# Optimization experiments

Measured on AMD Instinct MI355X. Metric: run time of the kernel, lower is better.

## Reference

```python
import jax, jax.numpy as jnp
import numpy as np

D_MODEL = 1024
N_HEADS = 16
HEAD_DIM = D_MODEL // N_HEADS


def setup_inputs() -> dict:
    key = jax.random.key(0)
    ks = jax.random.split(key, 12)
    B, S = 1, 4096
    s = 1.0 / np.sqrt(D_MODEL)
    return {
        "query": jax.random.normal(ks[0], (B, S, D_MODEL), jnp.float32),
        "key": jax.random.normal(ks[1], (B, S, D_MODEL), jnp.float32),
        "value": jax.random.normal(ks[2], (B, S, D_MODEL), jnp.float32),
        "attention_mask": jnp.ones((B, S), jnp.int32),
        "Wq": jax.random.normal(ks[3], (D_MODEL, D_MODEL), jnp.float32) * s,
        "bq": jax.random.normal(ks[4], (D_MODEL,), jnp.float32) * s,
        "Wk": jax.random.normal(ks[5], (D_MODEL, D_MODEL), jnp.float32) * s,
        "bk": jax.random.normal(ks[6], (D_MODEL,), jnp.float32) * s,
        "Wv": jax.random.normal(ks[7], (D_MODEL, D_MODEL), jnp.float32) * s,
        "bv": jax.random.normal(ks[8], (D_MODEL,), jnp.float32) * s,
        "Wo": jax.random.normal(ks[9], (D_MODEL, D_MODEL), jnp.float32) * s,
        "bo": jax.random.normal(ks[10], (D_MODEL,), jnp.float32) * s,
    }


def reference(query, key, value, attention_mask, Wq, bq, Wk, bk, Wv, bv, Wo, bo):
    B = query.shape[0]

    def split_heads(x):  # [B,S,D] -> [B,H,S,Dh]
        return x.reshape(B, -1, N_HEADS, HEAD_DIM).transpose(0, 2, 1, 3)

    q = split_heads(query @ Wq + bq)
    k = split_heads(key @ Wk + bk)
    v = split_heads(value @ Wv + bv)

    scores = jnp.einsum("bhqd,bhkd->bhqk", q, k) / np.sqrt(HEAD_DIM)
    # 2D mask [B, Skv] -> [B,1,1,Skv]; 0 positions filled with -1e9
    mask = attention_mask[:, None, None, :]
    scores = jnp.where(mask == 0, jnp.float32(-1e9), scores)
    weights = jax.nn.softmax(scores, axis=-1)
    out = jnp.einsum("bhqk,bhkd->bhqd", weights, v)
    out = out.transpose(0, 2, 1, 3).reshape(B, -1, D_MODEL)
    return out @ Wo + bo
```

## Files before the change

kernel.cpp:

```cpp
#include <hip/hip_runtime.h>
#include <hip/hip_bf16.h>
#include <cstdint>

typedef __attribute__((ext_vector_type(8))) short short8;
typedef __attribute__((ext_vector_type(4))) float floatx4;
typedef unsigned short u16;

#define D_MODEL 1024
#define S_LEN 4096
#define N_HEADS 16
#define HEAD_DIM 64

__device__ __forceinline__ u16 f2bf(float x) {
    union { float f; uint32_t u; } v; v.f = x;
    uint32_t u = v.u;
    u += 0x7fffu + ((u >> 16) & 1u);
    return (u16)(u >> 16);
}

__device__ __forceinline__ void load_lds16(const u16* g, u16* l) {
    __builtin_amdgcn_global_load_lds(
        (const __attribute__((address_space(1))) uint32_t*)g,
        (__attribute__((address_space(3))) uint32_t*)l, 16, 0, 0);
}

struct Conv3 { const float* s[3]; u16* d[3]; };
__global__ __launch_bounds__(256) void convert3(Conv3 a, int n4) {
    const int z = blockIdx.y;
    const float* __restrict__ src = a.s[z];
    u16* __restrict__ dst = a.d[z];
    int i = blockIdx.x * 256 + threadIdx.x;
    if (i >= n4) return;
    float4 v = reinterpret_cast<const float4*>(src)[i];
    ushort4 o;
    o.x = f2bf(v.x); o.y = f2bf(v.y); o.z = f2bf(v.z); o.w = f2bf(v.w);
    reinterpret_cast<ushort4*>(dst)[i] = o;
}

struct Tr4 { const float* s[4]; u16* d[4]; };
__global__ __launch_bounds__(256) void transpose4(Tr4 a, int R, int C) {
    __shared__ u16 tile[32][34];
    const int z = blockIdx.z;
    const float* __restrict__ in = a.s[z];
    u16* __restrict__ out = a.d[z];
    const int tx = threadIdx.x, ty = threadIdx.y;
    const int c0 = blockIdx.x * 32, r0 = blockIdx.y * 32;
    #pragma unroll
    for (int j = 0; j < 32; j += 8)
        tile[ty + j][tx] = f2bf(in[(size_t)(r0 + ty + j) * C + c0 + tx]);
    __syncthreads();
    #pragma unroll
    for (int j = 0; j < 32; j += 8)
        out[(size_t)(c0 + ty + j) * R + r0 + tx] = tile[tx][ty + j];
}

template <typename OutT>
__device__ __forceinline__ void gemm_bt_core(const u16* __restrict__ A, const u16* __restrict__ Bt,
                                             const float* __restrict__ bias, OutT* __restrict__ C,
                                             int M, int N, int K, int bx, int by, int trC) {
    constexpr int LDT = 72;
    __shared__ u16 As[128 * LDT];
    __shared__ u16 Bs[128 * LDT];
    const int tid = threadIdx.x;
    const int wave = tid >> 6, lane = tid & 63;
    const int quad = lane >> 4, n16 = lane & 15;
    const int wm = wave >> 1, wn = wave & 1;
    const int m0 = by * 128, n0 = bx * 128;

    floatx4 acc[4][4];
    #pragma unroll
    for (int i = 0; i < 4; ++i)
        #pragma unroll
        for (int t = 0; t < 4; ++t) acc[i][t] = (floatx4)0.f;

    for (int kt = 0; kt < K; kt += 64) {
        __syncthreads();
        #pragma unroll
        for (int u = 0; u < 4; ++u) {
            const int c = tid + u * 256;
            const int row = c >> 3, off = (c & 7) * 8;
            *reinterpret_cast<float4*>(&As[row * LDT + off]) =
                *reinterpret_cast<const float4*>(&A[(size_t)(m0 + row) * K + kt + off]);
            *reinterpret_cast<float4*>(&Bs[row * LDT + off]) =
                *reinterpret_cast<const float4*>(&Bt[(size_t)(n0 + row) * K + kt + off]);
        }
        __syncthreads();
        #pragma unroll
        for (int kk = 0; kk < 2; ++kk) {
            short8 a[4], b[4];
            #pragma unroll
            for (int i = 0; i < 4; ++i)
                a[i] = *reinterpret_cast<const short8*>(&As[(wm * 64 + i * 16 + n16) * LDT + kk * 32 + quad * 8]);
            #pragma unroll
            for (int t = 0; t < 4; ++t)
                b[t] = *reinterpret_cast<const short8*>(&Bs[(wn * 64 + t * 16 + n16) * LDT + kk * 32 + quad * 8]);
            #pragma unroll
            for (int i = 0; i < 4; ++i)
                #pragma unroll
                for (int t = 0; t < 4; ++t)
                    acc[i][t] = __builtin_amdgcn_mfma_f32_16x16x32_bf16(a[i], b[t], acc[i][t], 0, 0, 0);
        }
    }
    #pragma unroll
    for (int t = 0; t < 4; ++t) {
        const int col = n0 + wn * 64 + t * 16 + n16;
        const float bv = bias[col];
        #pragma unroll
        for (int i = 0; i < 4; ++i) {
            #pragma unroll
            for (int r = 0; r < 4; ++r) {
                const int row = m0 + wm * 64 + i * 16 + quad * 4 + r;
                const float val = acc[i][t][r] + bv;
                const size_t idx = trC ? ((size_t)col * M + row) : ((size_t)row * N + col);
                if constexpr (sizeof(OutT) == 2) C[idx] = f2bf(val);
                else                             C[idx] = val;
            }
        }
    }
}

struct QkvArgs {
    const u16* A[3]; const u16* B[3]; const float* bias[3]; u16* C[3];
};

__global__ __launch_bounds__(256) void gemm_qkv(QkvArgs args, int M, int N, int K) {
    const int z = blockIdx.z;
    gemm_bt_core<u16>(args.A[z], args.B[z], args.bias[z], args.C[z], M, N, K,
                      blockIdx.x, blockIdx.y, z == 2 ? 1 : 0);
}

__global__ __launch_bounds__(256) void gemm_out(const u16* __restrict__ A, const u16* __restrict__ Bt,
                                                const float* __restrict__ bias, float* __restrict__ C,
                                                int M, int N, int K) {
    gemm_bt_core<float>(A, Bt, bias, C, M, N, K, blockIdx.x, blockIdx.y, 0);
}

#define LDP 72
__global__ __launch_bounds__(256) void flash_attn(const u16* __restrict__ Q, const u16* __restrict__ Kb,
                                                  const u16* __restrict__ Vt, const int* __restrict__ mask,
                                                  u16* __restrict__ O) {
    __shared__ u16 Ks[2][64 * 64];
    __shared__ u16 Vs[2][64 * 64];
    __shared__ u16 Ps[4][16 * LDP];
    const int tid = threadIdx.x;
    const int wave = tid >> 6, lane = tid & 63;
    const int quad = lane >> 4, n16 = lane & 15;
    const int bid = blockIdx.x;
    const int h = (bid & 7) * 2 + ((bid >> 3) & 1);
    const int qt = bid >> 4;
    const int hd = h * HEAD_DIM;
    const int q0 = qt * 64 + wave * 16;

    const int rl = lane >> 3, cl = lane & 7;

    short8 b_q[2];
    #pragma unroll
    for (int kk = 0; kk < 2; ++kk)
        b_q[kk] = *reinterpret_cast<const short8*>(
            &Q[(size_t)(q0 + n16) * D_MODEL + hd + kk * 32 + quad * 8]);

    float l_i = 0.f;
    floatx4 o_acc[4];
    #pragma unroll
    for (int t = 0; t < 4; ++t) o_acc[t] = (floatx4)0.f;

    #pragma unroll
    for (int u = 0; u < 2; ++u) {
        const int r = wave * 16 + u * 8 + rl;
        const int c = cl ^ (r & 7);
        load_lds16(&Kb[(size_t)(0 + r) * D_MODEL + hd + c * 8], &Ks[0][(wave * 16 + u * 8) * 64]);
        load_lds16(&Vt[(size_t)(hd + r) * S_LEN + 0 + c * 8], &Vs[0][(wave * 16 + u * 8) * 64]);
    }

    for (int it = 0; it < 64; ++it) {
        const int cur = it & 1;
        const int k0 = it * 64;
        __syncthreads();

        const int kn = ((it + 1) & 63) * 64;
        #pragma unroll
        for (int u = 0; u < 2; ++u) {
            const int r = wave * 16 + u * 8 + rl;
            const int c = cl ^ (r & 7);
            load_lds16(&Kb[(size_t)(kn + r) * D_MODEL + hd + c * 8],
                       &Ks[cur ^ 1][(wave * 16 + u * 8) * 64]);
            load_lds16(&Vt[(size_t)(hd + r) * S_LEN + kn + c * 8],
                       &Vs[cur ^ 1][(wave * 16 + u * 8) * 64]);
        }

        floatx4 s[4];
        #pragma unroll
        for (int t = 0; t < 4; ++t) {
            s[t] = (floatx4)0.f;
            #pragma unroll
            for (int kk = 0; kk < 2; ++kk) {
                const int sw = ((kk * 4 + quad) ^ (n16 & 7)) * 8;
                short8 ak = *reinterpret_cast<const short8*>(&Ks[cur][(t * 16 + n16) * 64 + sw]);
                s[t] = __builtin_amdgcn_mfma_f32_16x16x32_bf16(ak, b_q[kk], s[t], 0, 0, 0);
            }
        }
        #pragma unroll
        for (int t = 0; t < 4; ++t) {
            const int4 mv = *reinterpret_cast<const int4*>(&mask[k0 + t * 16 + quad * 4]);
            const float p0 = __expf(fmaf(s[t][0], 0.125f, mv.x == 0 ? -1.0e9f : 0.f));
            const float p1 = __expf(fmaf(s[t][1], 0.125f, mv.y == 0 ? -1.0e9f : 0.f));
            const float p2 = __expf(fmaf(s[t][2], 0.125f, mv.z == 0 ? -1.0e9f : 0.f));
            const float p3 = __expf(fmaf(s[t][3], 0.125f, mv.w == 0 ? -1.0e9f : 0.f));
            l_i += (p0 + p1) + (p2 + p3);
            union { __hip_bfloat162 h; uint32_t u; } pa, pb;
            pa.h = __float22bfloat162_rn(make_float2(p0, p1));
            pb.h = __float22bfloat162_rn(make_float2(p2, p3));
            uint2 w; w.x = pa.u; w.y = pb.u;
            *reinterpret_cast<uint2*>(&Ps[wave][n16 * LDP + t * 16 + quad * 4]) = w;
        }
        asm volatile("s_waitcnt lgkmcnt(0)" ::: "memory");
        short8 ap[2];
        #pragma unroll
        for (int kkv = 0; kkv < 2; ++kkv)
            ap[kkv] = *reinterpret_cast<const short8*>(&Ps[wave][n16 * LDP + kkv * 32 + quad * 8]);
        asm volatile("" ::: "memory");
        #pragma unroll
        for (int t = 0; t < 4; ++t) {
            #pragma unroll
            for (int kkv = 0; kkv < 2; ++kkv) {
                const int sw = ((kkv * 4 + quad) ^ (n16 & 7)) * 8;
                short8 bv = *reinterpret_cast<const short8*>(&Vs[cur][(t * 16 + n16) * 64 + sw]);
                o_acc[t] = __builtin_amdgcn_mfma_f32_16x16x32_bf16(ap[kkv], bv, o_acc[t], 0, 0, 0);
            }
        }
    }
    float lt = l_i;
    lt += __shfl_xor(lt, 16);
    lt += __shfl_xor(lt, 32);
    const float inv_l = 1.f / lt;
    float lir[4];
    #pragma unroll
    for (int r = 0; r < 4; ++r) lir[r] = __shfl(inv_l, quad * 4 + r);
    #pragma unroll
    for (int t = 0; t < 4; ++t)
        #pragma unroll
        for (int r = 0; r < 4; ++r)
            O[(size_t)(q0 + quad * 4 + r) * D_MODEL + hd + t * 16 + n16] =
                f2bf(o_acc[t][r] * lir[r]);
}

extern "C" void kernel_launch(void* const* d_in, const int* in_sizes, int n_in,
                              void* d_out, int out_size, void* d_ws, size_t ws_size,
                              hipStream_t stream) {
    const float* query = (const float*)d_in[0];
    const float* key   = (const float*)d_in[1];
    const float* value = (const float*)d_in[2];
    const int*   mask  = (const int*)d_in[3];
    const float* Wq = (const float*)d_in[4];
    const float* bq = (const float*)d_in[5];
    const float* Wk = (const float*)d_in[6];
    const float* bk = (const float*)d_in[7];
    const float* Wv = (const float*)d_in[8];
    const float* bv = (const float*)d_in[9];
    const float* Wo = (const float*)d_in[10];
    const float* bo = (const float*)d_in[11];
    float* out = (float*)d_out;

    char* ws = (char*)d_ws;
    const size_t SZ_SD = (size_t)S_LEN * D_MODEL * 2;
    const size_t SZ_W  = (size_t)D_MODEL * D_MODEL * 2;
    u16* qb  = (u16*)(ws);
    u16* kb  = (u16*)(ws + SZ_SD);
    u16* vb  = (u16*)(ws + 2 * SZ_SD);
    u16* Wqt = (u16*)(ws + 3 * SZ_SD);
    u16* Wkt = (u16*)(ws + 3 * SZ_SD + SZ_W);
    u16* Wvt = (u16*)(ws + 3 * SZ_SD + 2 * SZ_W);
    u16* Wot = (u16*)(ws + 3 * SZ_SD + 3 * SZ_W);
    u16* Qp  = (u16*)(ws + 3 * SZ_SD + 4 * SZ_W);
    u16* Kp  = (u16*)(ws + 4 * SZ_SD + 4 * SZ_W);
    u16* Vpt = (u16*)(ws + 5 * SZ_SD + 4 * SZ_W);
    u16* Oa  = kb;

    const int n4 = S_LEN * D_MODEL / 4;
    Conv3 cv;
    cv.s[0] = query; cv.s[1] = key; cv.s[2] = value;
    cv.d[0] = qb;    cv.d[1] = kb;  cv.d[2] = vb;
    convert3<<<dim3(n4 / 256, 3), 256, 0, stream>>>(cv, n4);

    Tr4 tr;
    tr.s[0] = Wq; tr.s[1] = Wk; tr.s[2] = Wv; tr.s[3] = Wo;
    tr.d[0] = Wqt; tr.d[1] = Wkt; tr.d[2] = Wvt; tr.d[3] = Wot;
    transpose4<<<dim3(32, 32, 4), dim3(32, 8), 0, stream>>>(tr, D_MODEL, D_MODEL);

    QkvArgs qa;
    qa.A[0] = qb;  qa.A[1] = kb;  qa.A[2] = vb;
    qa.B[0] = Wqt; qa.B[1] = Wkt; qa.B[2] = Wvt;
    qa.bias[0] = bq; qa.bias[1] = bk; qa.bias[2] = bv;
    qa.C[0] = Qp; qa.C[1] = Kp; qa.C[2] = Vpt;
    gemm_qkv<<<dim3(8, 32, 3), 256, 0, stream>>>(qa, S_LEN, D_MODEL, D_MODEL);

    flash_attn<<<dim3(1024), 256, 0, stream>>>(Qp, Kp, Vpt, mask, Oa);

    gemm_out<<<dim3(8, 32), 256, 0, stream>>>(Oa, Wot, bo, out, S_LEN, D_MODEL, D_MODEL);
}
```

Baseline: 344.4 us.

## Swizzle GEMM and P tiles, async LDS loads, precomputed additive mask with exp2

The GEMM core now stages A/B tiles into unpadded, XOR-swizzled LDS through direct global-to-LDS loads instead of register round-trips. Flash attention writes and reads its P buffer with the same swizzle rather than padding, and unrolls the loop by two so the double-buffer index is a compile-time constant. A small new kernel turns the integer mask into an additive float mask, so the attention loop does one fma plus a hardware exp2 with the log2e folded into the scale. The aim is fewer LDS bank conflicts, less register staging, and cheaper softmax math, at the cost of one extra tiny launch.

```diff
diff --git a/kernel.cpp b/kernel.cpp
--- a/kernel.cpp
+++ b/kernel.cpp
@@ -10,6 +10,7 @@
 #define S_LEN 4096
 #define N_HEADS 16
 #define HEAD_DIM 64
+#define SCALE_LOG2E 0.18033688f
 
 __device__ __forceinline__ u16 f2bf(float x) {
     union { float f; uint32_t u; } v; v.f = x;
@@ -37,6 +38,19 @@
     reinterpret_cast<ushort4*>(dst)[i] = o;
 }
 
+__global__ __launch_bounds__(256) void mask_to_madd(const int* __restrict__ m,
+                                                    float* __restrict__ o, int n4) {
+    int i = blockIdx.x * 256 + threadIdx.x;
+    if (i >= n4) return;
+    int4 mv = reinterpret_cast<const int4*>(m)[i];
+    float4 f;
+    f.x = mv.x == 0 ? -1.0e30f : 0.f;
+    f.y = mv.y == 0 ? -1.0e30f : 0.f;
+    f.z = mv.z == 0 ? -1.0e30f : 0.f;
+    f.w = mv.w == 0 ? -1.0e30f : 0.f;
+    reinterpret_cast<float4*>(o)[i] = f;
+}
+
 struct Tr4 { const float* s[4]; u16* d[4]; };
 __global__ __launch_bounds__(256) void transpose4(Tr4 a, int R, int C) {
     __shared__ u16 tile[32][34];
@@ -58,14 +72,14 @@
 __device__ __forceinline__ void gemm_bt_core(const u16* __restrict__ A, const u16* __restrict__ Bt,
                                              const float* __restrict__ bias, OutT* __restrict__ C,
                                              int M, int N, int K, int bx, int by, int trC) {
-    constexpr int LDT = 72;
-    __shared__ u16 As[128 * LDT];
-    __shared__ u16 Bs[128 * LDT];
+    __shared__ u16 As[128 * 64];
+    __shared__ u16 Bs[128 * 64];
     const int tid = threadIdx.x;
     const int wave = tid >> 6, lane = tid & 63;
     const int quad = lane >> 4, n16 = lane & 15;
     const int wm = wave >> 1, wn = wave & 1;
     const int m0 = by * 128, n0 = bx * 128;
+    const int rl = lane >> 3, cl = lane & 7;
 
     floatx4 acc[4][4];
     #pragma unroll
@@ -77,23 +91,27 @@
         __syncthreads();
         #pragma unroll
         for (int u = 0; u < 4; ++u) {
-            const int c = tid + u * 256;
-            const int row = c >> 3, off = (c & 7) * 8;
-            *reinterpret_cast<float4*>(&As[row * LDT + off]) =
-                *reinterpret_cast<const float4*>(&A[(size_t)(m0 + row) * K + kt + off]);
-            *reinterpret_cast<float4*>(&Bs[row * LDT + off]) =
-                *reinterpret_cast<const float4*>(&Bt[(size_t)(n0 + row) * K + kt + off]);
+            const int r = wave * 32 + u * 8 + rl;
+            const int c = cl ^ (rl & 7);
+            load_lds16(&A[(size_t)(m0 + r) * K + kt + c * 8], &As[(wave * 32 + u * 8) * 64]);
+            load_lds16(&Bt[(size_t)(n0 + r) * K + kt + c * 8], &Bs[(wave * 32 + u * 8) * 64]);
         }
         __syncthreads();
         #pragma unroll
         for (int kk = 0; kk < 2; ++kk) {
             short8 a[4], b[4];
             #pragma unroll
-            for (int i = 0; i < 4; ++i)
-                a[i] = *reinterpret_cast<const short8*>(&As[(wm * 64 + i * 16 + n16) * LDT + kk * 32 + quad * 8]);
-            #pragma unroll
-            for (int t = 0; t < 4; ++t)
-                b[t] = *reinterpret_cast<const short8*>(&Bs[(wn * 64 + t * 16 + n16) * LDT + kk * 32 + quad * 8]);
+            for (int i = 0; i < 4; ++i) {
+                const int row = wm * 64 + i * 16 + n16;
+                const int sw = ((kk * 4 + quad) ^ (n16 & 7)) * 8;
+                a[i] = *reinterpret_cast<const short8*>(&As[row * 64 + sw]);
+            }
+            #pragma unroll
+            for (int t = 0; t < 4; ++t) {
+                const int row = wn * 64 + t * 16 + n16;
+                const int sw = ((kk * 4 + quad) ^ (n16 & 7)) * 8;
+                b[t] = *reinterpret_cast<const short8*>(&Bs[row * 64 + sw]);
+            }
             #pragma unroll
             for (int i = 0; i < 4; ++i)
                 #pragma unroll
@@ -135,13 +153,13 @@
     gemm_bt_core<float>(A, Bt, bias, C, M, N, K, blockIdx.x, blockIdx.y, 0);
 }
 
-#define LDP 72
 __global__ __launch_bounds__(256) void flash_attn(const u16* __restrict__ Q, const u16* __restrict__ Kb,
-                                                  const u16* __restrict__ Vt, const int* __restrict__ mask,
+                                                  const u16* __restrict__ Vt,
+                                                  const float* __restrict__ madd,
                                                   u16* __restrict__ O) {
     __shared__ u16 Ks[2][64 * 64];
     __shared__ u16 Vs[2][64 * 64];
-    __shared__ u16 Ps[4][16 * LDP];
+    __shared__ u16 Ps[4][16 * 64];
     const int tid = threadIdx.x;
     const int wave = tid >> 6, lane = tid & 63;
     const int quad = lane >> 4, n16 = lane & 15;
@@ -152,6 +170,7 @@
     const int q0 = qt * 64 + wave * 16;
 
     const int rl = lane >> 3, cl = lane & 7;
+    const int swz = n16 & 7;
 
     short8 b_q[2];
     #pragma unroll
@@ -167,65 +186,73 @@
     #pragma unroll
     for (int u = 0; u < 2; ++u) {
         const int r = wave * 16 + u * 8 + rl;
-        const int c = cl ^ (r & 7);
-        load_lds16(&Kb[(size_t)(0 + r) * D_MODEL + hd + c * 8], &Ks[0][(wave * 16 + u * 8) * 64]);
-        load_lds16(&Vt[(size_t)(hd + r) * S_LEN + 0 + c * 8], &Vs[0][(wave * 16 + u * 8) * 64]);
+        const int c = cl ^ (rl & 7);
+        load_lds16(&Kb[(size_t)r * D_MODEL + hd + c * 8], &Ks[0][(wave * 16 + u * 8) * 64]);
+        load_lds16(&Vt[(size_t)(hd + r) * S_LEN + c * 8], &Vs[0][(wave * 16 + u * 8) * 64]);
     }
 
-    for (int it = 0; it < 64; ++it) {
-        const int cur = it & 1;
-        const int k0 = it * 64;
-        __syncthreads();
-
-        const int kn = ((it + 1) & 63) * 64;
-        #pragma unroll
-        for (int u = 0; u < 2; ++u) {
-            const int r = wave * 16 + u * 8 + rl;
-            const int c = cl ^ (r & 7);
-            load_lds16(&Kb[(size_t)(kn + r) * D_MODEL + hd + c * 8],
-                       &Ks[cur ^ 1][(wave * 16 + u * 8) * 64]);
-            load_lds16(&Vt[(size_t)(hd + r) * S_LEN + kn + c * 8],
-                       &Vs[cur ^ 1][(wave * 16 + u * 8) * 64]);
-        }
-
-        floatx4 s[4];
-        #pragma unroll
-        for (int t = 0; t < 4; ++t) {
-            s[t] = (floatx4)0.f;
-            #pragma unroll
-            for (int kk = 0; kk < 2; ++kk) {
-                const int sw = ((kk * 4 + quad) ^ (n16 & 7)) * 8;
-                short8 ak = *reinterpret_cast<const short8*>(&Ks[cur][(t * 16 + n16) * 64 + sw]);
-                s[t] = __builtin_amdgcn_mfma_f32_16x16x32_bf16(ak, b_q[kk], s[t], 0, 0, 0);
-            }
-        }
-        #pragma unroll
-        for (int t = 0; t < 4; ++t) {
-            const int4 mv = *reinterpret_cast<const int4*>(&mask[k0 + t * 16 + quad * 4]);
-            const float p0 = __expf(fmaf(s[t][0], 0.125f, mv.x == 0 ? -1.0e9f : 0.f));
-            const float p1 = __expf(fmaf(s[t][1], 0.125f, mv.y == 0 ? -1.0e9f : 0.f));
-            const float p2 = __expf(fmaf(s[t][2], 0.125f, mv.z == 0 ? -1.0e9f : 0.f));
-            const float p3 = __expf(fmaf(s[t][3], 0.125f, mv.w == 0 ? -1.0e9f : 0.f));
-            l_i += (p0 + p1) + (p2 + p3);
-            union { __hip_bfloat162 h; uint32_t u; } pa, pb;
-            pa.h = __float22bfloat162_rn(make_float2(p0, p1));
-            pb.h = __float22bfloat162_rn(make_float2(p2, p3));
-            uint2 w; w.x = pa.u; w.y = pb.u;
-            *reinterpret_cast<uint2*>(&Ps[wave][n16 * LDP + t * 16 + quad * 4]) = w;
-        }
-        asm volatile("s_waitcnt lgkmcnt(0)" ::: "memory");
-        short8 ap[2];
-        #pragma unroll
-        for (int kkv = 0; kkv < 2; ++kkv)
-            ap[kkv] = *reinterpret_cast<const short8*>(&Ps[wave][n16 * LDP + kkv * 32 + quad * 8]);
-        asm volatile("" ::: "memory");
-        #pragma unroll
-        for (int t = 0; t < 4; ++t) {
-            #pragma unroll
-            for (int kkv = 0; kkv < 2; ++kkv) {
-                const int sw = ((kkv * 4 + quad) ^ (n16 & 7)) * 8;
-                short8 bv = *reinterpret_cast<const short8*>(&Vs[cur][(t * 16 + n16) * 64 + sw]);
-                o_acc[t] = __builtin_amdgcn_mfma_f32_16x16x32_bf16(ap[kkv], bv, o_acc[t], 0, 0, 0);
+    #pragma unroll 1
+    for (int it2 = 0; it2 < 32; ++it2) {
+        #pragma unroll
+        for (int half = 0; half < 2; ++half) {
+            const int it = it2 * 2 + half;
+            const int cur = half;
+            const int k0 = it * 64;
+            __syncthreads();
+
+            const int kn = ((it + 1) & 63) * 64;
+            #pragma unroll
+            for (int u = 0; u < 2; ++u) {
+                const int r = wave * 16 + u * 8 + rl;
+                const int c = cl ^ (rl & 7);
+                load_lds16(&Kb[(size_t)(kn + r) * D_MODEL + hd + c * 8],
+                           &Ks[cur ^ 1][(wave * 16 + u * 8) * 64]);
+                load_lds16(&Vt[(size_t)(hd + r) * S_LEN + kn + c * 8],
+                           &Vs[cur ^ 1][(wave * 16 + u * 8) * 64]);
+            }
+
+            floatx4 s[4];
+            #pragma unroll
+            for (int t = 0; t < 4; ++t) {
+                s[t] = (floatx4)0.f;
+                #pragma unroll
+                for (int kk = 0; kk < 2; ++kk) {
+                    const int sw = ((kk * 4 + quad) ^ swz) * 8;
+                    short8 ak = *reinterpret_cast<const short8*>(&Ks[cur][(t * 16 + n16) * 64 + sw]);
+                    s[t] = __builtin_amdgcn_mfma_f32_16x16x32_bf16(ak, b_q[kk], s[t], 0, 0, 0);
+                }
+            }
+            #pragma unroll
+            for (int t = 0; t < 4; ++t) {
+                const float4 mv = *reinterpret_cast<const float4*>(&madd[k0 + t * 16 + quad * 4]);
+                const float p0 = __builtin_amdgcn_exp2f(fmaf(s[t][0], SCALE_LOG2E, mv.x));
+                const float p1 = __builtin_amdgcn_exp2f(fmaf(s[t][1], SCALE_LOG2E, mv.y));
+                const float p2 = __builtin_amdgcn_exp2f(fmaf(s[t][2], SCALE_LOG2E, mv.z));
+                const float p3 = __builtin_amdgcn_exp2f(fmaf(s[t][3], SCALE_LOG2E, mv.w));
+                l_i += (p0 + p1) + (p2 + p3);
+                union { __hip_bfloat162 h; uint32_t u; } pa, pb;
+                pa.h = __float22bfloat162_rn(make_float2(p0, p1));
+                pb.h = __float22bfloat162_rn(make_float2(p2, p3));
+                uint2 w; w.x = pa.u; w.y = pb.u;
+                const int cw = t * 2 + (quad >> 1);
+                *reinterpret_cast<uint2*>(
+                    &Ps[wave][n16 * 64 + ((cw ^ swz) * 8 + (quad & 1) * 4)]) = w;
+            }
+            asm volatile("s_waitcnt lgkmcnt(0)" ::: "memory");
+            short8 ap[2];
+            #pragma unroll
+            for (int kkv = 0; kkv < 2; ++kkv)
+                ap[kkv] = *reinterpret_cast<const short8*>(
+                    &Ps[wave][n16 * 64 + ((kkv * 4 + quad) ^ swz) * 8]);
+            asm volatile("" ::: "memory");
+            #pragma unroll
+            for (int t = 0; t < 4; ++t) {
+                #pragma unroll
+                for (int kkv = 0; kkv < 2; ++kkv) {
+                    const int sw = ((kkv * 4 + quad) ^ swz) * 8;
+                    short8 bv = *reinterpret_cast<const short8*>(&Vs[cur][(t * 16 + n16) * 64 + sw]);
+                    o_acc[t] = __builtin_amdgcn_mfma_f32_16x16x32_bf16(ap[kkv], bv, o_acc[t], 0, 0, 0);
+                }
             }
         }
     }
@@ -274,6 +301,7 @@
     u16* Qp  = (u16*)(ws + 3 * SZ_SD + 4 * SZ_W);
     u16* Kp  = (u16*)(ws + 4 * SZ_SD + 4 * SZ_W);
     u16* Vpt = (u16*)(ws + 5 * SZ_SD + 4 * SZ_W);
+    float* maddf = (float*)(ws + 6 * SZ_SD + 4 * SZ_W);
     u16* Oa  = kb;
 
     const int n4 = S_LEN * D_MODEL / 4;
@@ -281,6 +309,8 @@
     cv.s[0] = query; cv.s[1] = key; cv.s[2] = value;
     cv.d[0] = qb;    cv.d[1] = kb;  cv.d[2] = vb;
     convert3<<<dim3(n4 / 256, 3), 256, 0, stream>>>(cv, n4);
+
+    mask_to_madd<<<dim3(4), 256, 0, stream>>>(mask, maddf, S_LEN / 4);
 
     Tr4 tr;
     tr.s[0] = Wq; tr.s[1] = Wk; tr.s[2] = Wv; tr.s[3] = Wo;
@@ -294,7 +324,7 @@
     qa.C[0] = Qp; qa.C[1] = Kp; qa.C[2] = Vpt;
     gemm_qkv<<<dim3(8, 32, 3), 256, 0, stream>>>(qa, S_LEN, D_MODEL, D_MODEL);
 
-    flash_attn<<<dim3(1024), 256, 0, stream>>>(Qp, Kp, Vpt, mask, Oa);
+    flash_attn<<<dim3(1024), 256, 0, stream>>>(Qp, Kp, Vpt, maddf, Oa);
 
     gemm_out<<<dim3(8, 32), 256, 0, stream>>>(Oa, Wot, bo, out, S_LEN, D_MODEL, D_MODEL);
 }
```

After: 319.9 us. 7.1% less time.
